# Kernel optimization log

Hardware: AMD Instinct MI355X
Metric: run time of the kernel (lower is better)

The kernel has to match this reference:

```python
import jax, jax.numpy as jnp
import numpy as np
import math

CHANNELS = 512
OUT_CHANNELS = 512
N_HEADS = 8
WINDOW = 4
K_CH = CHANNELS // N_HEADS


def _conv1x1(x, W, b):
    # x: (B, C_in, T), W: (C_out, C_in), b: (C_out,)
    return jnp.einsum('oc,bct->bot', W, x) + b[None, :, None]


def _get_relative_embeddings(emb, length, window=WINDOW):
    # emb: (H, 2*window+1, k_ch) -> (H, 2*length-1, k_ch)
    pad_length = max(length - (window + 1), 0)
    start = max(window + 1 - length, 0)
    e = jnp.pad(emb, ((0, 0), (pad_length, pad_length), (0, 0))) if pad_length > 0 else emb
    return e[:, start:start + 2 * length - 1]


def _relative_to_absolute(x):
    # x: (B, H, L, 2L-1) -> (B, H, L, L)
    b, h, L, _ = x.shape
    x = jnp.pad(x, ((0, 0), (0, 0), (0, 0), (0, 1)))          # (B,H,L,2L)
    xf = x.reshape(b, h, L * 2 * L)
    xf = jnp.pad(xf, ((0, 0), (0, 0), (L - 1, 0)))
    return xf.reshape(b, h, L + 1, 2 * L - 1)[:, :, :L, L - 1:]


def _absolute_to_relative(x):
    # x: (B, H, L, L) -> (B, H, L, 2L-1)
    b, h, L, _ = x.shape
    x = jnp.pad(x, ((0, 0), (0, 0), (0, 0), (0, L - 1)))       # (B,H,L,2L-1)
    xf = x.reshape(b, h, L * (2 * L - 1))
    xf = jnp.pad(xf, ((0, 0), (0, 0), (L, 0)))
    return xf.reshape(b, h, L, 2 * L)[:, :, :, 1:]


def setup_inputs() -> dict:
    key = jax.random.key(0)
    ks = jax.random.split(key, 16)
    B, C, T = 4, CHANNELS, 1024
    xavier = math.sqrt(2.0 / (C + C))
    rel_std = K_CH ** -0.5
    return {
        'x_q': jax.random.normal(ks[0], (B, C, T), jnp.float32),
        'x_k': jax.random.normal(ks[1], (B, C, T), jnp.float32),
        'x_v': jax.random.normal(ks[2], (B, C, T), jnp.float32),
        'Wq': jax.random.normal(ks[3], (C, C), jnp.float32) * xavier,
        'bq': jnp.zeros((C,), jnp.float32),
        'Wk': jax.random.normal(ks[4], (C, C), jnp.float32) * xavier,
        'bk': jnp.zeros((C,), jnp.float32),
        'Wv': jax.random.normal(ks[5], (C, C), jnp.float32) * xavier,
        'bv': jnp.zeros((C,), jnp.float32),
        'Wo': jax.random.normal(ks[6], (OUT_CHANNELS, C), jnp.float32) * xavier,
        'bo': jnp.zeros((OUT_CHANNELS,), jnp.float32),
        'emb_rel_k': jax.random.normal(ks[7], (N_HEADS, 2 * WINDOW + 1, K_CH), jnp.float32) * rel_std,
        'emb_rel_v': jax.random.normal(ks[8], (N_HEADS, 2 * WINDOW + 1, K_CH), jnp.float32) * rel_std,
    }


def reference(x_q, x_k, x_v, Wq, bq, Wk, bk, Wv, bv, Wo, bo, emb_rel_k, emb_rel_v):
    q = _conv1x1(x_q, Wq, bq)
    k = _conv1x1(x_k, Wk, bk)
    v = _conv1x1(x_v, Wv, bv)
    B, C, T = q.shape
    # (B, C, T) -> (B, H, T, k_ch); head h owns contiguous k_ch channel chunk
    qh = q.reshape(B, N_HEADS, K_CH, T).transpose(0, 1, 3, 2) / math.sqrt(K_CH)
    kh = k.reshape(B, N_HEADS, K_CH, T).transpose(0, 1, 3, 2)
    vh = v.reshape(B, N_HEADS, K_CH, T).transpose(0, 1, 3, 2)
    scores = jnp.einsum('bhtd,bhsd->bhts', qh, kh)              # (B,H,T,T)
    rel_k = _get_relative_embeddings(emb_rel_k, T)              # (H,2T-1,d)
    rel_logits = jnp.einsum('bhtd,hmd->bhtm', qh, rel_k)        # (B,H,T,2T-1)
    scores = scores + _relative_to_absolute(rel_logits)
    attn = jax.nn.softmax(scores, axis=-1)
    ctx = jnp.einsum('bhts,bhsd->bhtd', attn, vh)
    rel_w = _absolute_to_relative(attn)                         # (B,H,T,2T-1)
    rel_v = _get_relative_embeddings(emb_rel_v, T)
    ctx = ctx + jnp.einsum('bhtm,hmd->bhtd', rel_w, rel_v)
    out = ctx.transpose(0, 1, 3, 2).reshape(B, C, T)
    return _conv1x1(out, Wo, bo)
```

## Files before the change

### kernel.cpp

```cpp
#include <hip/hip_runtime.h>

#define T_LEN 1024
#define NH 8
#define DH 64
#define CCH 512
#define LOG2E 1.44269504088896340736f

typedef _Float16 f16;
typedef _Float16 f16x8 __attribute__((ext_vector_type(8)));
typedef _Float16 f16x4 __attribute__((ext_vector_type(4)));
typedef float f32x4 __attribute__((ext_vector_type(4)));

__device__ __forceinline__ void dma16(const void* g, void* l)
{
    __builtin_amdgcn_global_load_lds((const __attribute__((address_space(1))) void*)g,
                                     (__attribute__((address_space(3))) void*)l, 16, 0, 0);
}

__global__ __launch_bounds__(256)
void prep_kernel(const float* __restrict__ x0, const float* __restrict__ x1,
                 const float* __restrict__ x2, const float* __restrict__ W0,
                 const float* __restrict__ W1, const float* __restrict__ W2,
                 const float* __restrict__ W3, f16* __restrict__ o0,
                 f16* __restrict__ o1, f16* __restrict__ o2, f16* __restrict__ w0,
                 f16* __restrict__ w1, f16* __restrict__ w2, f16* __restrict__ w3,
                 int B)
{
    const int z = blockIdx.z;
    if (z < 3 * B) {
        const int t0 = blockIdx.x * 64, c0 = blockIdx.y * 64;
        const int which = z / B, b = z % B;
        const float* x = (which == 0) ? x0 : (which == 1) ? x1 : x2;
        f16* o = (which == 0) ? o0 : (which == 1) ? o1 : o2;

        __shared__ float L[64 * 68];
        const int cl = threadIdx.x & 63, g = threadIdx.x >> 6;
        const float* src = x + ((size_t)(b * CCH + c0 + cl)) * T_LEN + t0 + g * 16;
        #pragma unroll
        for (int j = 0; j < 4; ++j)
            *(float4*)&L[cl * 68 + g * 16 + 4 * j] = *(const float4*)&src[4 * j];
        __syncthreads();
        const int tl = threadIdx.x & 63, cg = (threadIdx.x >> 6) * 16;
        f16 h[16];
        #pragma unroll
        for (int j = 0; j < 16; ++j) h[j] = (f16)L[(cg + j) * 68 + tl];
        f16* dst = o + ((size_t)(b * T_LEN + t0 + tl)) * CCH + c0 + cg;
        *(f16x8*)&dst[0] = *(f16x8*)&h[0];
        *(f16x8*)&dst[8] = *(f16x8*)&h[8];
    } else {
        const int slice = z - 3 * B;
        size_t i = ((size_t)(slice * 128 + blockIdx.y * 16 + blockIdx.x) * 256 + threadIdx.x) * 4;
        const int wi = (int)(i >> 18);
        const size_t off = i & 262143;
        const float* src = (wi == 0) ? W0 : (wi == 1) ? W1 : (wi == 2) ? W2 : W3;
        f16* dst = (wi == 0) ? w0 : (wi == 1) ? w1 : (wi == 2) ? w2 : w3;
        float4 v4 = *(const float4*)&src[off];
        f16x4 h = {(f16)v4.x, (f16)v4.y, (f16)v4.z, (f16)v4.w};
        *(f16x4*)&dst[off] = h;
    }
}

__global__ __launch_bounds__(256)
void proj_qkv(const f16* __restrict__ xq, const f16* __restrict__ xk,
              const f16* __restrict__ xv, const f16* __restrict__ wq,
              const f16* __restrict__ wk, const f16* __restrict__ wv,
              const float* __restrict__ bq, const float* __restrict__ bk,
              const float* __restrict__ bv, f16* __restrict__ qo,
              f16* __restrict__ ko, f16* __restrict__ vo)
{
    const int which = blockIdx.z;
    const f16* X = (which == 0) ? xq : (which == 1) ? xk : xv;
    const f16* W = (which == 0) ? wq : (which == 1) ? wk : wv;
    const float* bias = (which == 0) ? bq : (which == 1) ? bk : bv;
    const float scale = (which == 0) ? 0.125f * LOG2E : 1.0f;

    const int r0 = blockIdx.x * 128;
    const int o0 = blockIdx.y * 64;
    const int tid = threadIdx.x;
    const int w = tid >> 6, lane = tid & 63;
    const int quad = lane >> 4, l15 = lane & 15;

    __shared__ __align__(16) f16 Ws[2][4096];

    const int srow = tid >> 3;
    const int scol = ((tid & 7) ^ (srow & 7)) << 3;
    const f16* Wg = W + (size_t)(o0 + srow) * CCH + scol;

    dma16(Wg, &Ws[0][(size_t)tid * 8]);
    dma16(Wg + (size_t)32 * CCH, &Ws[0][((size_t)tid + 256) * 8]);

    const f16* xp = X + (size_t)(r0 + 32 * w + l15) * CCH + quad * 8;
    f16x8 xf[2][2];
    #pragma unroll
    for (int ks = 0; ks < 2; ++ks)
        #pragma unroll
        for (int im = 0; im < 2; ++im)
            xf[ks][im] = *(const f16x8*)&xp[(size_t)(16 * im) * CCH + ks * 32];

    f32x4 acc[8] = {};

    for (int kc = 0; kc < 8; ++kc) {
        __syncthreads();
        if (kc < 7) {
            const int bf = (kc + 1) & 1, c1 = (kc + 1) * 64;
            dma16(Wg + c1, &Ws[bf][(size_t)tid * 8]);
            dma16(Wg + c1 + (size_t)32 * CCH, &Ws[bf][((size_t)tid + 256) * 8]);
        }
        const int nk = ((kc + 1) & 7) * 64;
        f16x8 xn[2][2];
        #pragma unroll
        for (int ks = 0; ks < 2; ++ks)
            #pragma unroll
            for (int im = 0; im < 2; ++im)
                xn[ks][im] = *(const f16x8*)&xp[(size_t)(16 * im) * CCH + nk + ks * 32];

        const int cb = kc & 1;
        #pragma unroll
        for (int ks = 0; ks < 2; ++ks) {
            const int sl = ((ks * 4 + quad) ^ (l15 & 7)) << 3;
            f16x8 wf[4];
            #pragma unroll
            for (int cm = 0; cm < 4; ++cm)
                wf[cm] = *(const f16x8*)&Ws[cb][(16 * cm + l15) * 64 + sl];
            if (which < 2) {
                #pragma unroll
                for (int im = 0; im < 2; ++im)
                    #pragma unroll
                    for (int cm = 0; cm < 4; ++cm)
                        acc[im * 4 + cm] = __builtin_amdgcn_mfma_f32_16x16x32_f16(
                            xf[ks][im], wf[cm], acc[im * 4 + cm], 0, 0, 0);
            } else {
                #pragma unroll
                for (int cm = 0; cm < 4; ++cm)
                    #pragma unroll
                    for (int in = 0; in < 2; ++in)
                        acc[cm * 2 + in] = __builtin_amdgcn_mfma_f32_16x16x32_f16(
                            wf[cm], xf[ks][in], acc[cm * 2 + in], 0, 0, 0);
            }
        }
        #pragma unroll
        for (int ks = 0; ks < 2; ++ks)
            #pragma unroll
            for (int im = 0; im < 2; ++im)
                xf[ks][im] = xn[ks][im];
    }

    if (which < 2) {
        f16* out = (which == 0) ? qo : ko;
        float bl[4];
        #pragma unroll
        for (int cm = 0; cm < 4; ++cm) bl[cm] = bias[o0 + 16 * cm + l15];
        #pragma unroll
        for (int im = 0; im < 2; ++im)
            #pragma unroll
            for (int r = 0; r < 4; ++r) {
                size_t row = (size_t)(r0 + 32 * w + 16 * im + 4 * quad + r) * CCH;
                #pragma unroll
                for (int cm = 0; cm < 4; ++cm)
                    out[row + o0 + 16 * cm + l15] =
                        (f16)((acc[im * 4 + cm][r] + bl[cm]) * scale);
            }
    } else {
        const int bb = r0 >> 10, tb = r0 & 1023;
        #pragma unroll
        for (int cm = 0; cm < 4; ++cm) {
            float4 bv4 = *(const float4*)&bias[o0 + 16 * cm + 4 * quad];
            float bl[4] = {bv4.x, bv4.y, bv4.z, bv4.w};
            #pragma unroll
            for (int r = 0; r < 4; ++r) {
                size_t row = ((size_t)(bb * CCH + o0 + 16 * cm + 4 * quad + r)) * T_LEN;
                #pragma unroll
                for (int in = 0; in < 2; ++in)
                    vo[row + tb + 32 * w + 16 * in + l15] =
                        (f16)(acc[cm * 2 + in][r] + bl[r]);
            }
        }
    }
}

__global__ __launch_bounds__(256)
void attn_mfma(const f16* __restrict__ q, const f16* __restrict__ kk,
               const f16* __restrict__ v, const float* __restrict__ ekg,
               const float* __restrict__ evg, f16* __restrict__ ctx)
{
    const int t0 = blockIdx.x * 64, h = blockIdx.y, b = blockIdx.z;
    const int tid = threadIdx.x;
    const int w = tid >> 6, lane = tid & 63;
    const int quad = lane >> 4, l15 = lane & 15;

    __shared__ __align__(16) f16 Qs[4096], Ps[4096];
    __shared__ __align__(16) f16 Ks[2][4096], Vs[2][4096];
    __shared__ float eks[576], evs[576];
    __shared__ float ls[64];

    const int srow = tid >> 3;
    const int scol = ((tid & 7) ^ (srow & 7)) << 3;

    for (int i = tid; i < 576; i += 256) {
        eks[i] = ekg[h * 576 + i];
        evs[i] = evg[h * 576 + i];
    }

    const f16* gk = kk + ((size_t)(b * T_LEN + srow)) * CCH + h * DH + scol;
    const f16* gv = v + ((size_t)(b * CCH + h * DH + srow)) * T_LEN + scol;

    dma16(q + ((size_t)(b * T_LEN + t0 + srow)) * CCH + h * DH + scol, &Qs[(size_t)tid * 8]);
    dma16(q + ((size_t)(b * T_LEN + t0 + srow + 32)) * CCH + h * DH + scol, &Qs[((size_t)tid + 256) * 8]);
    dma16(gk, &Ks[0][(size_t)tid * 8]);
    dma16(gk + (size_t)32 * CCH, &Ks[0][((size_t)tid + 256) * 8]);
    dma16(gv, &Vs[0][(size_t)tid * 8]);
    dma16(gv + (size_t)32 * T_LEN, &Vs[0][((size_t)tid + 256) * 8]);
    __syncthreads();

    f16x8 qf[2];
    #pragma unroll
    for (int ks = 0; ks < 2; ++ks)
        qf[ks] = *(const f16x8*)&Qs[(16 * w + l15) * 64 + (((ks * 4 + quad) ^ (l15 & 7)) << 3)];

    const int myt = 16 * w + l15;
    float Ssum = 0.f;
    f32x4 O[4] = {};

    const bool corner_hi = (blockIdx.x == 0);
    const bool corner_lo = (blockIdx.x == 15);

    for (int it = 0; it < 16; ++it) {
        const int kb = it, cb = it & 1;
        if (it) __syncthreads();

        if (it < 15) {
            const int nb = cb ^ 1;
            dma16(gk + (size_t)((it + 1) * 64) * CCH, &Ks[nb][(size_t)tid * 8]);
            dma16(gk + (size_t)((it + 1) * 64 + 32) * CCH, &Ks[nb][((size_t)tid + 256) * 8]);
            dma16(gv + (it + 1) * 64, &Vs[nb][(size_t)tid * 8]);
            dma16(gv + (size_t)32 * T_LEN + (it + 1) * 64, &Vs[nb][((size_t)tid + 256) * 8]);
        }

        f32x4 S[4] = {};
        #pragma unroll
        for (int ks = 0; ks < 2; ++ks) {
            #pragma unroll
            for (int ct = 0; ct < 4; ++ct) {
                f16x8 a = *(const f16x8*)&Ks[cb][(16 * ct + l15) * 64 + (((ks * 4 + quad) ^ (l15 & 7)) << 3)];
                S[ct] = __builtin_amdgcn_mfma_f32_16x16x32_f16(a, qf[ks], S[ct], 0, 0, 0);
            }
        }

        if ((corner_hi && kb == 15) || (corner_lo && kb == 0)) {
            const int s0g = kb * 64;
            #pragma unroll
            for (int ct = 0; ct < 4; ++ct)
                #pragma unroll
                for (int r = 0; r < 4; ++r) {
                    int t_g = t0 + myt;
                    int s_g = s0g + 16 * ct + 4 * quad + r;
                    int df = s_g - t_g;
                    if (df >= 1019 && df <= 1023) {
                        const float* ekp = &eks[(df - 1019) * 64];
                        float sacc = 0.f;
                        for (int d = 0; d < 64; ++d)
                            sacc += (float)Qs[myt * 64 + (((d >> 3) ^ (myt & 7)) << 3) + (d & 7)] * ekp[d];
                        S[ct][r] += sacc;
                    } else if (df >= -1023 && df <= -1021) {
                        const float* ekp = &eks[(1029 + df) * 64];
                        const int t2 = myt - 1;
                        float sacc = 0.f;
                        for (int d = 0; d < 64; ++d)
                            sacc += (float)Qs[t2 * 64 + (((d >> 3) ^ (t2 & 7)) << 3) + (d & 7)] * ekp[d];
                        S[ct][r] += sacc;
                    }
                }
        }

        #pragma unroll
        for (int ct = 0; ct < 4; ++ct) {
            f16x4 pk_;
            #pragma unroll
            for (int r = 0; r < 4; ++r) {
                float p = exp2f(S[ct][r]);
                Ssum += p;
                pk_[r] = (f16)p;
            }
            int colh = (((2 * ct + (quad >> 1)) ^ (myt & 7)) << 3) + (quad & 1) * 4;
            *(f16x4*)&Ps[myt * 64 + colh] = pk_;
        }

        #pragma unroll
        for (int ks = 0; ks < 2; ++ks) {
            f16x8 a = *(const f16x8*)&Ps[(16 * w + l15) * 64 + (((ks * 4 + quad) ^ (l15 & 7)) << 3)];
            #pragma unroll
            for (int ct = 0; ct < 4; ++ct) {
                f16x8 bf = *(const f16x8*)&Vs[cb][(16 * ct + l15) * 64 + (((ks * 4 + quad) ^ (l15 & 7)) << 3)];
                O[ct] = __builtin_amdgcn_mfma_f32_16x16x32_f16(a, bf, O[ct], 0, 0, 0);
            }
        }

        const int s0g = kb * 64;
        if (s0g <= t0 + 67 && s0g + 63 >= t0 - 4) {
            #pragma unroll
            for (int r = 0; r < 4; ++r) {
                int t_loc = 16 * w + 4 * quad + r;
                int t_g = t0 + t_loc;
                int slo = max(s0g, t_g - 4), shi = min(s0g + 63, t_g + 4);
                for (int s = slo; s <= shi; ++s) {
                    int sl = s - s0g;
                    float p = (float)Ps[t_loc * 64 + (((sl >> 3) ^ (t_loc & 7)) << 3) + (sl & 7)];
                    const float* evp = &evs[(s - t_g + 4) * 64];
                    #pragma unroll
                    for (int ct = 0; ct < 4; ++ct)
                        O[ct][r] += p * evp[16 * ct + l15];
                }
            }
        }
    }

    Ssum += __shfl_xor(Ssum, 16);
    Ssum += __shfl_xor(Ssum, 32);
    if (quad == 0) ls[myt] = 1.0f / Ssum;
    __syncthreads();

    #pragma unroll
    for (int r = 0; r < 4; ++r) {
        const int t_loc = 16 * w + 4 * quad + r;
        const float rl = ls[t_loc];
        size_t rowo = ((size_t)(b * T_LEN + t0 + t_loc)) * CCH + h * DH;
        #pragma unroll
        for (int ct = 0; ct < 4; ++ct)
            ctx[rowo + 16 * ct + l15] = (f16)(O[ct][r] * rl);
    }
}

__global__ __launch_bounds__(256)
void proj_out(const f16* __restrict__ ctx, const f16* __restrict__ Wo,
              const float* __restrict__ bo, float* __restrict__ out)
{
    const int r0 = blockIdx.x * 64;
    const int o0 = blockIdx.y * 64;
    const int tid = threadIdx.x;
    const int w = tid >> 6, lane = tid & 63;
    const int quad = lane >> 4, l15 = lane & 15;

    __shared__ __align__(16) f16 Ws[2][4096];

    const int srow = tid >> 3;
    const int scol = ((tid & 7) ^ (srow & 7)) << 3;
    const f16* Wg = Wo + (size_t)(o0 + srow) * CCH + scol;

    dma16(Wg, &Ws[0][(size_t)tid * 8]);
    dma16(Wg + (size_t)32 * CCH, &Ws[0][((size_t)tid + 256) * 8]);

    const f16* cp = ctx + (size_t)(r0 + 16 * w + l15) * CCH + quad * 8;
    f16x8 cf[2];
    #pragma unroll
    for (int ks = 0; ks < 2; ++ks)
        cf[ks] = *(const f16x8*)&cp[ks * 32];

    f32x4 acc[4] = {};

    for (int kc = 0; kc < 8; ++kc) {
        __syncthreads();
        if (kc < 7) {
            const int bf = (kc + 1) & 1, c1 = (kc + 1) * 64;
            dma16(Wg + c1, &Ws[bf][(size_t)tid * 8]);
            dma16(Wg + c1 + (size_t)32 * CCH, &Ws[bf][((size_t)tid + 256) * 8]);
        }
        const int nk = ((kc + 1) & 7) * 64;
        f16x8 cn[2];
        #pragma unroll
        for (int ks = 0; ks < 2; ++ks)
            cn[ks] = *(const f16x8*)&cp[nk + ks * 32];

        const int cb = kc & 1;
        #pragma unroll
        for (int ks = 0; ks < 2; ++ks) {
            const int sl = ((ks * 4 + quad) ^ (l15 & 7)) << 3;
            #pragma unroll
            for (int cm = 0; cm < 4; ++cm) {
                f16x8 wf = *(const f16x8*)&Ws[cb][(16 * cm + l15) * 64 + sl];
                acc[cm] = __builtin_amdgcn_mfma_f32_16x16x32_f16(wf, cf[ks], acc[cm], 0, 0, 0);
            }
        }
        cf[0] = cn[0];
        cf[1] = cn[1];
    }

    const int bb = r0 >> 10, tb = r0 & 1023;
    #pragma unroll
    for (int cm = 0; cm < 4; ++cm) {
        float4 bv4 = *(const float4*)&bo[o0 + 16 * cm + 4 * quad];
        float bl[4] = {bv4.x, bv4.y, bv4.z, bv4.w};
        #pragma unroll
        for (int r = 0; r < 4; ++r) {
            size_t row = ((size_t)(bb * CCH + o0 + 16 * cm + 4 * quad + r)) * T_LEN;
            out[row + tb + 16 * w + l15] = acc[cm][r] + bl[r];
        }
    }
}

extern "C" void kernel_launch(void* const* d_in, const int* in_sizes, int n_in,
                              void* d_out, int out_size, void* d_ws, size_t ws_size,
                              hipStream_t stream)
{
    const float* x_q = (const float*)d_in[0];
    const float* x_k = (const float*)d_in[1];
    const float* x_v = (const float*)d_in[2];
    const float* Wq  = (const float*)d_in[3];
    const float* bq  = (const float*)d_in[4];
    const float* Wk  = (const float*)d_in[5];
    const float* bk  = (const float*)d_in[6];
    const float* Wv  = (const float*)d_in[7];
    const float* bv  = (const float*)d_in[8];
    const float* Wo  = (const float*)d_in[9];
    const float* bo  = (const float*)d_in[10];
    const float* erk = (const float*)d_in[11];
    const float* erv = (const float*)d_in[12];

    const int B = in_sizes[0] / (CCH * T_LEN);
    const size_t te = (size_t)B * CCH * T_LEN;
    const size_t we = (size_t)CCH * CCH;

    f16* p = (f16*)d_ws;
    f16* xTq = p; p += te;
    f16* xTk = p; p += te;
    f16* xTv = p; p += te;
    f16* wqh = p; p += we;
    f16* wkh = p; p += we;
    f16* wvh = p; p += we;
    f16* woh = p; p += we;
    f16* qh  = p; p += te;
    f16* kh  = p; p += te;
    f16* vh  = p; p += te;
    f16* ch  = p; p += te;

    dim3 blk(256);
    prep_kernel<<<dim3(16, 8, 3 * B + 8), blk, 0, stream>>>(
        x_q, x_k, x_v, Wq, Wk, Wv, Wo, xTq, xTk, xTv, wqh, wkh, wvh, woh, B);
    proj_qkv<<<dim3(B * 8, 8, 3), blk, 0, stream>>>(
        xTq, xTk, xTv, wqh, wkh, wvh, bq, bk, bv, qh, kh, vh);
    attn_mfma<<<dim3(T_LEN / 64, NH, B), blk, 0, stream>>>(
        qh, kh, vh, erk, erv, ch);
    proj_out<<<dim3(B * 16, 8), blk, 0, stream>>>(
        ch, woh, bo, (float*)d_out);
}
```

Measured before the change: 152.7 us.

## Fuse fp32-to-fp16 weight conversion into projection kernels' LDS staging

The separate weight-conversion slice of the prep kernel is removed. The projection kernels now load fp32 weights directly, convert them in registers and write swizzled fp16 tiles to LDS, replacing the async global-to-LDS DMA. This drops one pass over the weights and the fp16 weight workspace, but each projection block re-reads and re-converts fp32 weights (twice the bytes) through registers instead of async DMA, which can reduce overlap. The relative-embedding tables in attention are also stored as fp16 in LDS.

```diff
diff --git a/kernel.cpp b/kernel.cpp
--- a/kernel.cpp
+++ b/kernel.cpp
@@ -19,58 +19,59 @@
 
 __global__ __launch_bounds__(256)
 void prep_kernel(const float* __restrict__ x0, const float* __restrict__ x1,
-                 const float* __restrict__ x2, const float* __restrict__ W0,
-                 const float* __restrict__ W1, const float* __restrict__ W2,
-                 const float* __restrict__ W3, f16* __restrict__ o0,
-                 f16* __restrict__ o1, f16* __restrict__ o2, f16* __restrict__ w0,
-                 f16* __restrict__ w1, f16* __restrict__ w2, f16* __restrict__ w3,
-                 int B)
+                 const float* __restrict__ x2, f16* __restrict__ o0,
+                 f16* __restrict__ o1, f16* __restrict__ o2, int B)
 {
     const int z = blockIdx.z;
-    if (z < 3 * B) {
-        const int t0 = blockIdx.x * 64, c0 = blockIdx.y * 64;
-        const int which = z / B, b = z % B;
-        const float* x = (which == 0) ? x0 : (which == 1) ? x1 : x2;
-        f16* o = (which == 0) ? o0 : (which == 1) ? o1 : o2;
-
-        __shared__ float L[64 * 68];
-        const int cl = threadIdx.x & 63, g = threadIdx.x >> 6;
-        const float* src = x + ((size_t)(b * CCH + c0 + cl)) * T_LEN + t0 + g * 16;
-        #pragma unroll
-        for (int j = 0; j < 4; ++j)
-            *(float4*)&L[cl * 68 + g * 16 + 4 * j] = *(const float4*)&src[4 * j];
-        __syncthreads();
-        const int tl = threadIdx.x & 63, cg = (threadIdx.x >> 6) * 16;
-        f16 h[16];
-        #pragma unroll
-        for (int j = 0; j < 16; ++j) h[j] = (f16)L[(cg + j) * 68 + tl];
-        f16* dst = o + ((size_t)(b * T_LEN + t0 + tl)) * CCH + c0 + cg;
-        *(f16x8*)&dst[0] = *(f16x8*)&h[0];
-        *(f16x8*)&dst[8] = *(f16x8*)&h[8];
-    } else {
-        const int slice = z - 3 * B;
-        size_t i = ((size_t)(slice * 128 + blockIdx.y * 16 + blockIdx.x) * 256 + threadIdx.x) * 4;
-        const int wi = (int)(i >> 18);
-        const size_t off = i & 262143;
-        const float* src = (wi == 0) ? W0 : (wi == 1) ? W1 : (wi == 2) ? W2 : W3;
-        f16* dst = (wi == 0) ? w0 : (wi == 1) ? w1 : (wi == 2) ? w2 : w3;
-        float4 v4 = *(const float4*)&src[off];
-        f16x4 h = {(f16)v4.x, (f16)v4.y, (f16)v4.z, (f16)v4.w};
-        *(f16x4*)&dst[off] = h;
-    }
+    const int t0 = blockIdx.x * 64, c0 = blockIdx.y * 64;
+    const int which = z / B, b = z % B;
+    const float* x = (which == 0) ? x0 : (which == 1) ? x1 : x2;
+    f16* o = (which == 0) ? o0 : (which == 1) ? o1 : o2;
+
+    __shared__ float L[64 * 68];
+    const int cl = threadIdx.x & 63, g = threadIdx.x >> 6;
+    const float* src = x + ((size_t)(b * CCH + c0 + cl)) * T_LEN + t0 + g * 16;
+    #pragma unroll
+    for (int j = 0; j < 4; ++j)
+        *(float4*)&L[cl * 68 + g * 16 + 4 * j] = *(const float4*)&src[4 * j];
+    __syncthreads();
+    const int tl = threadIdx.x & 63, cg = (threadIdx.x >> 6) * 16;
+    f16 h[16];
+    #pragma unroll
+    for (int j = 0; j < 16; ++j) h[j] = (f16)L[(cg + j) * 68 + tl];
+    f16* dst = o + ((size_t)(b * T_LEN + t0 + tl)) * CCH + c0 + cg;
+    *(f16x8*)&dst[0] = *(f16x8*)&h[0];
+    *(f16x8*)&dst[8] = *(f16x8*)&h[8];
+}
+
+__device__ __forceinline__ void stage_w_fp32(const float* __restrict__ Wg,
+                                             int c1, f16* __restrict__ dstbuf,
+                                             int wrow, int wc)
+{
+    float4 a = *(const float4*)&Wg[c1 + 0];
+    float4 b = *(const float4*)&Wg[c1 + 4];
+    float4 c = *(const float4*)&Wg[c1 + 8];
+    float4 d = *(const float4*)&Wg[c1 + 12];
+    f16 hh[16] = {(f16)a.x, (f16)a.y, (f16)a.z, (f16)a.w,
+                  (f16)b.x, (f16)b.y, (f16)b.z, (f16)b.w,
+                  (f16)c.x, (f16)c.y, (f16)c.z, (f16)c.w,
+                  (f16)d.x, (f16)d.y, (f16)d.z, (f16)d.w};
+    const int cg0 = (wc >> 3);
+    *(f16x8*)&dstbuf[wrow * 64 + ((cg0 ^ (wrow & 7)) << 3)]       = *(f16x8*)&hh[0];
+    *(f16x8*)&dstbuf[wrow * 64 + (((cg0 + 1) ^ (wrow & 7)) << 3)] = *(f16x8*)&hh[8];
 }
 
 __global__ __launch_bounds__(256)
 void proj_qkv(const f16* __restrict__ xq, const f16* __restrict__ xk,
-              const f16* __restrict__ xv, const f16* __restrict__ wq,
-              const f16* __restrict__ wk, const f16* __restrict__ wv,
+              const f16* __restrict__ xv, const float* __restrict__ wq,
+              const float* __restrict__ wk, const float* __restrict__ wv,
               const float* __restrict__ bq, const float* __restrict__ bk,
               const float* __restrict__ bv, f16* __restrict__ qo,
               f16* __restrict__ ko, f16* __restrict__ vo)
 {
     const int which = blockIdx.z;
     const f16* X = (which == 0) ? xq : (which == 1) ? xk : xv;
-    const f16* W = (which == 0) ? wq : (which == 1) ? wk : wv;
+    const float* W = (which == 0) ? wq : (which == 1) ? wk : wv;
     const float* bias = (which == 0) ? bq : (which == 1) ? bk : bv;
     const float scale = (which == 0) ? 0.125f * LOG2E : 1.0f;
 
@@ -82,12 +83,11 @@
 
     __shared__ __align__(16) f16 Ws[2][4096];
 
-    const int srow = tid >> 3;
-    const int scol = ((tid & 7) ^ (srow & 7)) << 3;
-    const f16* Wg = W + (size_t)(o0 + srow) * CCH + scol;
-
-    dma16(Wg, &Ws[0][(size_t)tid * 8]);
-    dma16(Wg + (size_t)32 * CCH, &Ws[0][((size_t)tid + 256) * 8]);
+    const int wrow = tid >> 2;
+    const int wc   = (tid & 3) * 16;
+    const float* Wg = W + (size_t)(o0 + wrow) * CCH + wc;
+
+    stage_w_fp32(Wg, 0, Ws[0], wrow, wc);
 
     const f16* xp = X + (size_t)(r0 + 32 * w + l15) * CCH + quad * 8;
     f16x8 xf[2][2];
@@ -101,11 +101,8 @@
 
     for (int kc = 0; kc < 8; ++kc) {
         __syncthreads();
-        if (kc < 7) {
-            const int bf = (kc + 1) & 1, c1 = (kc + 1) * 64;
-            dma16(Wg + c1, &Ws[bf][(size_t)tid * 8]);
-            dma16(Wg + c1 + (size_t)32 * CCH, &Ws[bf][((size_t)tid + 256) * 8]);
-        }
+        if (kc < 7)
+            stage_w_fp32(Wg, (kc + 1) * 64, Ws[(kc + 1) & 1], wrow, wc);
         const int nk = ((kc + 1) & 7) * 64;
         f16x8 xn[2][2];
         #pragma unroll
@@ -190,15 +187,15 @@
 
     __shared__ __align__(16) f16 Qs[4096], Ps[4096];
     __shared__ __align__(16) f16 Ks[2][4096], Vs[2][4096];
-    __shared__ float eks[576], evs[576];
+    __shared__ f16 eks[576], evs[576];
     __shared__ float ls[64];
 
     const int srow = tid >> 3;
     const int scol = ((tid & 7) ^ (srow & 7)) << 3;
 
     for (int i = tid; i < 576; i += 256) {
-        eks[i] = ekg[h * 576 + i];
-        evs[i] = evg[h * 576 + i];
+        eks[i] = (f16)ekg[h * 576 + i];
+        evs[i] = (f16)evg[h * 576 + i];
     }
 
     const f16* gk = kk + ((size_t)(b * T_LEN + srow)) * CCH + h * DH + scol;
@@ -256,17 +253,17 @@
                     int s_g = s0g + 16 * ct + 4 * quad + r;
                     int df = s_g - t_g;
                     if (df >= 1019 && df <= 1023) {
-                        const float* ekp = &eks[(df - 1019) * 64];
+                        const f16* ekp = &eks[(df - 1019) * 64];
                         float sacc = 0.f;
                         for (int d = 0; d < 64; ++d)
-                            sacc += (float)Qs[myt * 64 + (((d >> 3) ^ (myt & 7)) << 3) + (d & 7)] * ekp[d];
+                            sacc += (float)Qs[myt * 64 + (((d >> 3) ^ (myt & 7)) << 3) + (d & 7)] * (float)ekp[d];
                         S[ct][r] += sacc;
                     } else if (df >= -1023 && df <= -1021) {
-                        const float* ekp = &eks[(1029 + df) * 64];
+                        const f16* ekp = &eks[(1029 + df) * 64];
                         const int t2 = myt - 1;
                         float sacc = 0.f;
                         for (int d = 0; d < 64; ++d)
-                            sacc += (float)Qs[t2 * 64 + (((d >> 3) ^ (t2 & 7)) << 3) + (d & 7)] * ekp[d];
+                            sacc += (float)Qs[t2 * 64 + (((d >> 3) ^ (t2 & 7)) << 3) + (d & 7)] * (float)ekp[d];
                         S[ct][r] += sacc;
                     }
                 }
@@ -305,10 +302,10 @@
                 for (int s = slo; s <= shi; ++s) {
                     int sl = s - s0g;
                     float p = (float)Ps[t_loc * 64 + (((sl >> 3) ^ (t_loc & 7)) << 3) + (sl & 7)];
-                    const float* evp = &evs[(s - t_g + 4) * 64];
+                    const f16* evp = &evs[(s - t_g + 4) * 64];
                     #pragma unroll
                     for (int ct = 0; ct < 4; ++ct)
-                        O[ct][r] += p * evp[16 * ct + l15];
+                        O[ct][r] += p * (float)evp[16 * ct + l15];
                 }
             }
         }
@@ -331,7 +328,7 @@
 }
 
 __global__ __launch_bounds__(256)
-void proj_out(const f16* __restrict__ ctx, const f16* __restrict__ Wo,
+void proj_out(const f16* __restrict__ ctx, const float* __restrict__ Wo,
               const float* __restrict__ bo, float* __restrict__ out)
 {
     const int r0 = blockIdx.x * 64;
@@ -342,12 +339,11 @@
 
     __shared__ __align__(16) f16 Ws[2][4096];
 
-    const int srow = tid >> 3;
-    const int scol = ((tid & 7) ^ (srow & 7)) << 3;
-    const f16* Wg = Wo + (size_t)(o0 + srow) * CCH + scol;
-
-    dma16(Wg, &Ws[0][(size_t)tid * 8]);
-    dma16(Wg + (size_t)32 * CCH, &Ws[0][((size_t)tid + 256) * 8]);
+    const int wrow = tid >> 2;
+    const int wc   = (tid & 3) * 16;
+    const float* Wg = Wo + (size_t)(o0 + wrow) * CCH + wc;
+
+    stage_w_fp32(Wg, 0, Ws[0], wrow, wc);
 
     const f16* cp = ctx + (size_t)(r0 + 16 * w + l15) * CCH + quad * 8;
     f16x8 cf[2];
@@ -359,11 +355,8 @@
 
     for (int kc = 0; kc < 8; ++kc) {
         __syncthreads();
-        if (kc < 7) {
-            const int bf = (kc + 1) & 1, c1 = (kc + 1) * 64;
-            dma16(Wg + c1, &Ws[bf][(size_t)tid * 8]);
-            dma16(Wg + c1 + (size_t)32 * CCH, &Ws[bf][((size_t)tid + 256) * 8]);
-        }
+        if (kc < 7)
+            stage_w_fp32(Wg, (kc + 1) * 64, Ws[(kc + 1) & 1], wrow, wc);
         const int nk = ((kc + 1) & 7) * 64;
         f16x8 cn[2];
         #pragma unroll
@@ -417,28 +410,23 @@
 
     const int B = in_sizes[0] / (CCH * T_LEN);
     const size_t te = (size_t)B * CCH * T_LEN;
-    const size_t we = (size_t)CCH * CCH;
 
     f16* p = (f16*)d_ws;
     f16* xTq = p; p += te;
     f16* xTk = p; p += te;
     f16* xTv = p; p += te;
-    f16* wqh = p; p += we;
-    f16* wkh = p; p += we;
-    f16* wvh = p; p += we;
-    f16* woh = p; p += we;
     f16* qh  = p; p += te;
     f16* kh  = p; p += te;
     f16* vh  = p; p += te;
     f16* ch  = p; p += te;
 
     dim3 blk(256);
-    prep_kernel<<<dim3(16, 8, 3 * B + 8), blk, 0, stream>>>(
-        x_q, x_k, x_v, Wq, Wk, Wv, Wo, xTq, xTk, xTv, wqh, wkh, wvh, woh, B);
+    prep_kernel<<<dim3(16, 8, 3 * B), blk, 0, stream>>>(
+        x_q, x_k, x_v, xTq, xTk, xTv, B);
     proj_qkv<<<dim3(B * 8, 8, 3), blk, 0, stream>>>(
-        xTq, xTk, xTv, wqh, wkh, wvh, bq, bk, bv, qh, kh, vh);
+        xTq, xTk, xTv, Wq, Wk, Wv, bq, bk, bv, qh, kh, vh);
     attn_mfma<<<dim3(T_LEN / 64, NH, B), blk, 0, stream>>>(
         qh, kh, vh, erk, erv, ch);
     proj_out<<<dim3(B * 16, 8), blk, 0, stream>>>(
-        ch, woh, bo, (float*)d_out);
-}
+        ch, Wo, bo, (float*)d_out);
+}
```

New measurement: 159.7 us. 1.05x slower.
